# Performance work log

Measured on AMD Instinct MI355X. Metric: run time of the kernel, lower is better.

## Reference

```python
import jax, jax.numpy as jnp
import numpy as np

HEADS = 16
DHEAD = 128
B, S, DMODEL = 2, 2048, 2048


def setup_inputs() -> dict:
    key = jax.random.key(0)
    k1, k2, k3 = jax.random.split(key, 3)
    x = jax.random.normal(k1, (B, S, DMODEL), dtype=jnp.float32)
    # Linear weights, stored as [in, out] so forward is x @ w (no bias).
    w_in = jax.random.normal(k2, (DMODEL, 3 * HEADS * DHEAD), dtype=jnp.float32) * (DMODEL ** -0.5)
    w_out = jax.random.normal(k3, (HEADS * DHEAD, DMODEL), dtype=jnp.float32) * ((HEADS * DHEAD) ** -0.5)
    # Causal mask: True = masked (strictly upper triangular), broadcast over batch & heads.
    mask = jnp.triu(jnp.ones((S, S), dtype=jnp.bool_), k=1)[None, None, :, :]
    return {"x": x, "w_in": w_in, "w_out": w_out, "mask": mask}


def reference(x, w_in, w_out, mask):
    b, s, _ = x.shape
    # Fused QKV projection: [b,s,3*H*dh] -> [b,s,H,3*dh] -> chunk into q,k,v [b,s,H,dh]
    projected = (x @ w_in).reshape(b, s, HEADS, 3 * DHEAD)
    q, k, v = jnp.split(projected, 3, axis=-1)
    # Scores [b,H,l,L], scaled by 1/sqrt(dhead)
    scale = 1.0 / (DHEAD ** 0.5)
    a = jnp.einsum("blhd,bLhd->bhlL", q, k) * scale
    a = jnp.where(mask, -jnp.inf, a)
    a = jax.nn.softmax(a, axis=-1)
    # Weighted values -> [b,l,H,dh] -> flatten heads -> output projection
    out = jnp.einsum("bhlL,bLhd->blhd", a, v).reshape(b, s, HEADS * DHEAD)
    return out @ w_out
```

## Files before the change

kernel.cpp:

```cpp
#include <hip/hip_runtime.h>

#define HD    16
#define DH    128
#define BB    2
#define SS    2048
#define DM    2048
#define NQKV  6144
#define MTOT  4096

typedef short   bfx8  __attribute__((ext_vector_type(8)));
typedef float   f32x4 __attribute__((ext_vector_type(4)));

__device__ __forceinline__ unsigned short f2bf(float f) {
  union { float f; unsigned int u; } c; c.f = f;
  unsigned int u = c.u + 0x7FFFu + ((c.u >> 16) & 1u);
  return (unsigned short)(u >> 16);
}

__device__ __forceinline__ void gload_lds16(const unsigned short* g, unsigned short* l) {
  __builtin_amdgcn_global_load_lds(
      (const __attribute__((address_space(1))) unsigned int*)g,
      (__attribute__((address_space(3))) unsigned int*)l, 16, 0, 0);
}

#define BARS() do { asm volatile("s_waitcnt lgkmcnt(0)" ::: "memory");               \
                    __builtin_amdgcn_sched_barrier(0); __builtin_amdgcn_s_barrier(); \
                    __builtin_amdgcn_sched_barrier(0); } while (0)
#define VMCNT10() do { asm volatile("s_waitcnt vmcnt(10)" ::: "memory"); \
                       __builtin_amdgcn_sched_barrier(0); } while (0)
#define VMCNT8() do { asm volatile("s_waitcnt vmcnt(8)" ::: "memory"); \
                      __builtin_amdgcn_sched_barrier(0); } while (0)

__global__ __launch_bounds__(256) void prep_fused_k(const float* __restrict__ x,
                                                    unsigned short* __restrict__ Xb,
                                                    const float* __restrict__ w_in,
                                                    unsigned short* __restrict__ Wit) {
  __shared__ float t[32][33];
  const int bid = (int)blockIdx.x;
  if (bid < 8192) {
    const int i = bid * 256 + (int)threadIdx.x;
    const float4 v = *(const float4*)(x + (size_t)i * 4);
    ushort4 o;
    o.x = f2bf(v.x); o.y = f2bf(v.y); o.z = f2bf(v.z); o.w = f2bf(v.w);
    *(ushort4*)(Xb + (size_t)i * 4) = o;
    return;
  }
  const int tb = bid - 8192;
  const int c0 = (tb % 192) * 32, r0 = (tb / 192) * 32;
  const int tx = threadIdx.x & 31, ty = threadIdx.x >> 5;
#pragma unroll
  for (int i = 0; i < 4; i++) {
    int r = r0 + ty + i * 8;
    t[ty + i * 8][tx] = w_in[(size_t)r * NQKV + c0 + tx];
  }
  __syncthreads();
#pragma unroll
  for (int i = 0; i < 4; i++) {
    int c = c0 + ty + i * 8;
    Wit[(size_t)c * DM + r0 + tx] = f2bf(t[tx][ty + i * 8]);
  }
}

__global__ __launch_bounds__(256, 2) void gemm128_qkv_k(const unsigned short* __restrict__ A,
                                                        const unsigned short* __restrict__ Bt,
                                                        unsigned short* __restrict__ Qg,
                                                        unsigned short* __restrict__ Kg,
                                                        unsigned short* __restrict__ Vg,
                                                        int K) {
  __shared__ __align__(16) unsigned short Asb[2][128 * 64];
  __shared__ __align__(16) unsigned short Bsb[2][192 * 64];
  const int tid = threadIdx.x;
  const int lane = tid & 63, wid = tid >> 6;
  const int wr = wid >> 1, wc = wid & 1;
  const int cbase = lane & 15, rgrp = lane >> 4;
  const int bid = (int)blockIdx.x;
  const int id = (bid & 7) * 128 + (bid >> 3);
  const int nb = id >> 5, mb = id & 31;
  const size_t m0 = (size_t)mb * 128, n0 = (size_t)nb * 192;
  const int nkt = K >> 6;

#define STAGE_A32(u_, g_) do {                                                          \
    const int uc_ = ((u_) < nkt ? (u_) : (nkt - 1));                                    \
    const int r_ = tid >> 3, s_ = tid & 7;                                              \
    gload_lds16(A + (m0 + (g_) * 32 + r_) * (size_t)K + uc_ * 64 +                      \
                    (((s_ * 16) ^ ((r_ & 7) << 4)) >> 1),                               \
                &Asb[(u_) & 1][(g_) * 2048] + tid * 8); } while (0)
#define STAGE_B32(u_, g_) do {                                                          \
    const int uc_ = ((u_) < nkt ? (u_) : (nkt - 1));                                    \
    const int r_ = tid >> 3, s_ = tid & 7;                                              \
    gload_lds16(Bt + (n0 + (g_) * 32 + r_) * (size_t)K + uc_ * 64 +                     \
                    (((s_ * 16) ^ ((r_ & 7) << 4)) >> 1),                               \
                &Bsb[(u_) & 1][(g_) * 2048] + tid * 8); } while (0)

  const int axor = (cbase & 7) << 4;
  int a_off[2], b_off[2];
#pragma unroll
  for (int ks = 0; ks < 2; ks++) {
    a_off[ks] = ((wr * 64 + cbase) * 128 + ((ks * 64 + rgrp * 16) ^ axor)) >> 1;
    b_off[ks] = ((wc * 96 + cbase) * 128 + ((ks * 64 + rgrp * 16) ^ axor)) >> 1;
  }

#define RD_AALL(dst_, p_) do { _Pragma("unroll")                                         \
    for (int mf_ = 0; mf_ < 4; mf_++) { _Pragma("unroll")                                \
      for (int ks_ = 0; ks_ < 2; ks_++)                                                  \
        dst_[mf_][ks_] = *(const bfx8*)((p_) + a_off[ks_] + mf_ * 1024); } } while (0)
#define RD_BP(dst_, p_, P_) do { _Pragma("unroll")                                       \
    for (int nf_ = 0; nf_ < 2; nf_++) { _Pragma("unroll")                                \
      for (int ks_ = 0; ks_ < 2; ks_++)                                                  \
        dst_[nf_][ks_] = *(const bfx8*)((p_) + b_off[ks_] + (nf_ + (P_)) * 1024); } } while (0)

#define MFMA_P(no_, AF_, BF_) do {                                                       \
    __builtin_amdgcn_s_setprio(1);                                                      \
    _Pragma("unroll")                                                                    \
    for (int mf_ = 0; mf_ < 4; mf_++) { _Pragma("unroll")                                \
      for (int nf_ = 0; nf_ < 2; nf_++) { _Pragma("unroll")                              \
        for (int ks_ = 0; ks_ < 2; ks_++)                                                \
          acc[mf_][nf_ + (no_)] = __builtin_amdgcn_mfma_f32_16x16x32_bf16(               \
              AF_[mf_][ks_], BF_[nf_][ks_], acc[mf_][nf_ + (no_)], 0, 0, 0); } }         \
    __builtin_amdgcn_s_setprio(0); } while (0)

  f32x4 acc[4][6];
  const f32x4 z = {0.f, 0.f, 0.f, 0.f};
#pragma unroll
  for (int mf = 0; mf < 4; mf++)
#pragma unroll
    for (int nf = 0; nf < 6; nf++) acc[mf][nf] = z;

  STAGE_A32(0, 0); STAGE_A32(0, 1); STAGE_A32(0, 2); STAGE_A32(0, 3);
  STAGE_B32(0, 0); STAGE_B32(0, 1); STAGE_B32(0, 2);
  STAGE_B32(0, 3); STAGE_B32(0, 4); STAGE_B32(0, 5);
  STAGE_A32(1, 0); STAGE_A32(1, 1); STAGE_A32(1, 2); STAGE_A32(1, 3);
  STAGE_B32(1, 0); STAGE_B32(1, 1); STAGE_B32(1, 2);
  STAGE_B32(1, 3); STAGE_B32(1, 4); STAGE_B32(1, 5);
  VMCNT10();
  BARS();
  bfx8 aA[4][2], b01A[2][2], aB[4][2], b01B[2][2];
  RD_AALL(aA, &Asb[0][0]);
  RD_BP(b01A, &Bsb[0][0], 0);
  BARS();

#define TILE_BODY(u_, Ac, B01c, An, B01n) do {                                           \
    const unsigned short* Bs_  = &Bsb[(u_) & 1][0];                                      \
    const unsigned short* Asn_ = &Asb[((u_) + 1) & 1][0];                                \
    const unsigned short* Bsn_ = &Bsb[((u_) + 1) & 1][0];                                \
    bfx8 b23[2][2], b45[2][2];                                                           \
        \
                                                             \
    RD_BP(b23, Bs_, 2);                                                                  \
    STAGE_A32((u_) + 2, 0); STAGE_A32((u_) + 2, 1);                                      \
    STAGE_A32((u_) + 2, 2); STAGE_A32((u_) + 2, 3);                                      \
    STAGE_B32((u_) + 2, 0); STAGE_B32((u_) + 2, 3);                                      \
    BARS();                                                                              \
    MFMA_P(0, Ac, B01c);                                                                 \
         \
    RD_BP(b45, Bs_, 4);                                                                  \
    STAGE_B32((u_) + 2, 1); STAGE_B32((u_) + 2, 4);                                      \
    BARS();                                                                              \
    MFMA_P(2, Ac, b23);                                                                  \
        \
                                           \
    STAGE_B32((u_) + 2, 2); STAGE_B32((u_) + 2, 5);                                      \
    VMCNT10();                                                                           \
    BARS();                                                                              \
    RD_AALL(An, Asn_);                                                                   \
    RD_BP(B01n, Bsn_, 0);                                                                \
    MFMA_P(4, Ac, b45);                                                                  \
    BARS();                                                                              \
  } while (0)

#pragma unroll 1
  for (int u = 0; u < nkt; u += 2) {
    TILE_BODY(u,     aA, b01A, aB, b01B);
    TILE_BODY(u + 1, aB, b01B, aA, b01A);
  }
#undef TILE_BODY
#undef STAGE_A32
#undef STAGE_B32

#pragma unroll
  for (int mf = 0; mf < 4; mf++)
#pragma unroll
    for (int nf = 0; nf < 6; nf++) {
      const int nn = (int)n0 + wc * 96 + nf * 16;
      const int h = nn / 384, tt = (nn >> 7) % 3;
      const int d = (nn & 127) + cbase;
      const int row0 = (int)m0 + wr * 64 + mf * 16 + rgrp * 4;
      const int bb = row0 >> 11;
      const int s0 = row0 & 2047;
      if (tt == 2) {
        ushort4 v;
        v.x = f2bf(acc[mf][nf][0]); v.y = f2bf(acc[mf][nf][1]);
        v.z = f2bf(acc[mf][nf][2]); v.w = f2bf(acc[mf][nf][3]);
        *(ushort4*)(Vg + ((size_t)(bb * HD + h) * DH + d) * SS + s0) = v;
      } else {
        unsigned short* dst = (tt == 0 ? Qg : Kg);
#pragma unroll
        for (int r = 0; r < 4; r++)
          dst[((size_t)(bb * HD + h) * SS + s0 + r) * DH + d] = f2bf(acc[mf][nf][r]);
      }
    }
}

__global__ __launch_bounds__(256, 2) void gemm128_out_k(const unsigned short* __restrict__ A,
                                                        const unsigned short* __restrict__ Bt,
                                                        float* __restrict__ C, int K, int ldc) {
  __shared__ __align__(16) unsigned short Asb[2][128 * 64];
  __shared__ __align__(16) unsigned short Bsb[2][128 * 64];
  const int tid = threadIdx.x;
  const int lane = tid & 63, wid = tid >> 6;
  const int wr = wid >> 1, wc = wid & 1;
  const int cbase = lane & 15, rgrp = lane >> 4;
  const int bid = (int)blockIdx.x;
  const int id = (bid & 7) * 64 + (bid >> 3);
  const int nb = id >> 5, mb = id & 31;
  const size_t m0 = (size_t)mb * 128, n0 = (size_t)nb * 128;
  const int nkt = K >> 6;

#define STAGE_AO32(u_, g_) do {                                                         \
    const int uc_ = ((u_) < nkt ? (u_) : (nkt - 1));                                    \
    const int r_ = tid >> 3, s_ = tid & 7;                                              \
    gload_lds16(A + (m0 + (g_) * 32 + r_) * (size_t)K + uc_ * 64 +                      \
                    (((s_ * 16) ^ ((r_ & 7) << 4)) >> 1),                               \
                &Asb[(u_) & 1][(g_) * 2048] + tid * 8); } while (0)
#define STAGE_BO32(u_, g_) do {                                                         \
    const int uc_ = ((u_) < nkt ? (u_) : (nkt - 1));                                    \
    const int r_ = tid >> 3, s_ = tid & 7;                                              \
    gload_lds16(Bt + (n0 + (g_) * 32 + r_) * (size_t)K + uc_ * 64 +                     \
                    (((s_ * 16) ^ ((r_ & 7) << 4)) >> 1),                               \
                &Bsb[(u_) & 1][(g_) * 2048] + tid * 8); } while (0)

  const int axor = (cbase & 7) << 4;
  int a_off[2], b_off[2];
#pragma unroll
  for (int ks = 0; ks < 2; ks++) {
    a_off[ks] = ((wr * 64 + cbase) * 128 + ((ks * 64 + rgrp * 16) ^ axor)) >> 1;
    b_off[ks] = ((wc * 64 + cbase) * 128 + ((ks * 64 + rgrp * 16) ^ axor)) >> 1;
  }

  f32x4 acc[4][4];
  const f32x4 z = {0.f, 0.f, 0.f, 0.f};
#pragma unroll
  for (int mf = 0; mf < 4; mf++)
#pragma unroll
    for (int nf = 0; nf < 4; nf++) acc[mf][nf] = z;

  STAGE_AO32(0, 0); STAGE_AO32(0, 1); STAGE_AO32(0, 2); STAGE_AO32(0, 3);
  STAGE_BO32(0, 0); STAGE_BO32(0, 1); STAGE_BO32(0, 2); STAGE_BO32(0, 3);
  STAGE_AO32(1, 0); STAGE_AO32(1, 1); STAGE_AO32(1, 2); STAGE_AO32(1, 3);
  STAGE_BO32(1, 0); STAGE_BO32(1, 1); STAGE_BO32(1, 2); STAGE_BO32(1, 3);
  VMCNT8();
  BARS();
  bfx8 aA[4][2], b01A[2][2], aB[4][2], b01B[2][2];
  RD_AALL(aA, &Asb[0][0]);
  RD_BP(b01A, &Bsb[0][0], 0);
  BARS();

#define TILE_BODY_Q(u_, Ac, B01c, An, B01n) do {                                         \
    const unsigned short* Bs_  = &Bsb[(u_) & 1][0];                                      \
    const unsigned short* Asn_ = &Asb[((u_) + 1) & 1][0];                                \
    const unsigned short* Bsn_ = &Bsb[((u_) + 1) & 1][0];                                \
    bfx8 b23[2][2];                                                                      \
        \
                                                             \
    RD_BP(b23, Bs_, 2);                                                                  \
    STAGE_AO32((u_) + 2, 0); STAGE_AO32((u_) + 2, 1);                                    \
    STAGE_AO32((u_) + 2, 2); STAGE_AO32((u_) + 2, 3);                                    \
    STAGE_BO32((u_) + 2, 0); STAGE_BO32((u_) + 2, 2);                                    \
    BARS();                                                                              \
    MFMA_P(0, Ac, B01c);                                                                 \
         \
                             \
    STAGE_BO32((u_) + 2, 1); STAGE_BO32((u_) + 2, 3);                                    \
    VMCNT8();                                                                            \
    BARS();                                                                              \
    RD_AALL(An, Asn_);                                                                   \
    RD_BP(B01n, Bsn_, 0);                                                                \
    MFMA_P(2, Ac, b23);                                                                  \
    BARS();                                                                              \
  } while (0)

#pragma unroll 1
  for (int u = 0; u < nkt; u += 2) {
    TILE_BODY_Q(u,     aA, b01A, aB, b01B);
    TILE_BODY_Q(u + 1, aB, b01B, aA, b01A);
  }
#undef TILE_BODY_Q
#undef STAGE_AO32
#undef STAGE_BO32

#pragma unroll
  for (int mf = 0; mf < 4; mf++)
#pragma unroll
    for (int nf = 0; nf < 4; nf++)
#pragma unroll
      for (int r = 0; r < 4; r++) {
        size_t row = m0 + wr * 64 + mf * 16 + rgrp * 4 + r;
        size_t col = n0 + wc * 64 + nf * 16 + cbase;
        C[row * ldc + col] = acc[mf][nf][r];
      }
}

__global__ __launch_bounds__(256) void attn_wot_k(const unsigned short* __restrict__ Qg,
                                                  const unsigned short* __restrict__ Kg,
                                                  const unsigned short* __restrict__ Vg,
                                                  unsigned short* __restrict__ ao,
                                                  const float* __restrict__ w_out,
                                                  unsigned short* __restrict__ Wot) {
  __shared__ __align__(16) unsigned short Klds[2][64 * 128];
  __shared__ __align__(16) unsigned short Vt[2][128 * 64];
  __shared__ __align__(16) unsigned short Plds[4][16 * 64];
  const int tid = threadIdx.x;
  const int bid = (int)blockIdx.x;

  if (bid >= 1024) {
    float* t = (float*)&Klds[0][0];
    const int tb = bid - 1024;
    const int c0 = (tb & 63) * 32, r0 = (tb >> 6) * 32;
    const int tx = tid & 31, ty = tid >> 5;
#pragma unroll
    for (int i = 0; i < 4; i++) {
      int r = r0 + ty + i * 8;
      t[(ty + i * 8) * 33 + tx] = w_out[(size_t)r * DM + c0 + tx];
    }
    __syncthreads();
#pragma unroll
    for (int i = 0; i < 4; i++) {
      int c = c0 + ty + i * 8;
      Wot[(size_t)c * DM + r0 + tx] = f2bf(t[tx * 33 + ty + i * 8]);
    }
    return;
  }

  const int lane = tid & 63, wid = tid >> 6;
  const int cbase = lane & 15, rgrp = lane >> 4;
  const int cx = (cbase & 7) << 4;

  const int bh = (bid & 7) * 4 + ((bid >> 3) & 3);
  const int qt = 31 - (bid >> 5);
  const int b = bh >> 4, h = bh & 15;
  const int qbase = qt * 64;

  const unsigned short* qp0 = Qg + (size_t)(b * HD + h) * SS * DH;
  const unsigned short* kp  = Kg + (size_t)(b * HD + h) * SS * DH;
  const unsigned short* vp  = Vg + (size_t)(b * HD + h) * DH * SS;
  const float scale = 0.08838834764831845f;
  const f32x4 z = {0.f, 0.f, 0.f, 0.f};
  const int qi = qbase + wid * 16 + cbase;

  bfx8 qf[4];
  {
    const unsigned short* qp = qp0 + (size_t)qi * DH;
#pragma unroll
    for (int ks = 0; ks < 4; ks++) qf[ks] = *(const bfx8*)(qp + ks * 32 + rgrp * 8);
  }

  float m_run = -1e30f, l_run = 0.f;
  f32x4 o[8];
#pragma unroll
  for (int mb = 0; mb < 8; mb++) o[mb] = z;

#define STAGE_T(t_, s_) do {                                                        \
    const int kvb_ = (t_) * 64;                                                     \
    _Pragma("unroll")                                                               \
    for (int i_ = 0; i_ < 4; i_++) {                                                \
      int idx_ = i_ * 256 + tid;                                                    \
      int r_ = idx_ >> 4, bo_ = (idx_ & 15) * 16;                                   \
      gload_lds16(kp + (size_t)(kvb_ + r_) * DH + ((bo_ ^ ((r_ & 7) << 4)) >> 1),   \
                  &Klds[s_][idx_ * 8]);                                             \
    }                                                                               \
    _Pragma("unroll")                                                               \
    for (int i_ = 0; i_ < 4; i_++) {                                                \
      int idx_ = i_ * 256 + tid;                                                    \
      int d_ = idx_ >> 3, bo_ = (idx_ & 7) * 16;                                    \
      gload_lds16(vp + (size_t)d_ * SS + kvb_ + ((bo_ ^ ((d_ & 7) << 4)) >> 1),     \
                  &Vt[s_][idx_ * 8]);                                               \
    } } while (0)

  const int ntiles = qt + 1;
  STAGE_T(0, 0);
  __syncthreads();

  for (int t = 0; t < ntiles; ++t) {
    const int sel = t & 1;
    if (t + 1 < ntiles) STAGE_T(t + 1, sel ^ 1);
    const unsigned short* Ks_ = &Klds[sel][0];
    const unsigned short* Vs_ = &Vt[sel][0];
    const int kvb = t * 64;

    f32x4 s[4];
#pragma unroll
    for (int mf = 0; mf < 4; mf++) s[mf] = z;
#pragma unroll
    for (int mf = 0; mf < 4; mf++)
#pragma unroll
      for (int ks = 0; ks < 4; ks++) {
        bfx8 kf = *(const bfx8*)(Ks_ + (((mf * 16 + cbase) * 256 + ((ks * 64 + rgrp * 16) ^ cx)) >> 1));
        s[mf] = __builtin_amdgcn_mfma_f32_16x16x32_bf16(kf, qf[ks], s[mf], 0, 0, 0);
      }

    float sv[4][4];
    const bool diag = (t == ntiles - 1);
#pragma unroll
    for (int mf = 0; mf < 4; mf++)
#pragma unroll
      for (int r = 0; r < 4; r++) {
        float v = s[mf][r] * scale;
        if (diag && (kvb + mf * 16 + rgrp * 4 + r > qi)) v = -1e30f;
        sv[mf][r] = v;
      }
    float tm = sv[0][0];
#pragma unroll
    for (int mf = 0; mf < 4; mf++)
#pragma unroll
      for (int r = 0; r < 4; r++) tm = fmaxf(tm, sv[mf][r]);
    tm = fmaxf(tm, __shfl_xor(tm, 16));
    tm = fmaxf(tm, __shfl_xor(tm, 32));
    const float mnew = fmaxf(m_run, tm);
    float p[4][4];
    float rs = 0.f;
#pragma unroll
    for (int mf = 0; mf < 4; mf++)
#pragma unroll
      for (int r = 0; r < 4; r++) { p[mf][r] = __expf(sv[mf][r] - mnew); rs += p[mf][r]; }
    rs += __shfl_xor(rs, 16);
    rs += __shfl_xor(rs, 32);
    const float alpha = __expf(m_run - mnew);
    l_run = l_run * alpha + rs;
    m_run = mnew;
#pragma unroll
    for (int mb = 0; mb < 8; mb++)
#pragma unroll
      for (int r = 0; r < 4; r++) o[mb][r] *= alpha;

#pragma unroll
    for (int mf = 0; mf < 4; mf++)
#pragma unroll
      for (int rr = 0; rr < 2; rr++) {
        unsigned int pp = (unsigned int)f2bf(p[mf][2 * rr]) |
                          ((unsigned int)f2bf(p[mf][2 * rr + 1]) << 16);
        *(unsigned int*)((char*)&Plds[wid][0] +
                         (cbase * 128 + ((mf * 32 + rgrp * 8 + rr * 4) ^ cx))) = pp;
      }
    bfx8 pf[2];
#pragma unroll
    for (int k2 = 0; k2 < 2; k2++)
      pf[k2] = *(const bfx8*)((const char*)&Plds[wid][0] +
                              (cbase * 128 + ((k2 * 64 + rgrp * 16) ^ cx)));

#pragma unroll
    for (int mb = 0; mb < 8; mb++)
#pragma unroll
      for (int k2 = 0; k2 < 2; k2++) {
        bfx8 vf = *(const bfx8*)(Vs_ + (((mb * 16 + cbase) * 128 + ((k2 * 64 + rgrp * 16) ^ cx)) >> 1));
        o[mb] = __builtin_amdgcn_mfma_f32_16x16x32_bf16(vf, pf[k2], o[mb], 0, 0, 0);
      }
    __syncthreads();
  }
#undef STAGE_T

  const float rinv = 1.0f / l_run;
  unsigned short* aop = ao + ((size_t)(b * SS + qi)) * DM + h * DH + rgrp * 4;
#pragma unroll
  for (int mb = 0; mb < 8; mb++) {
    ushort4 v;
    v.x = f2bf(o[mb][0] * rinv); v.y = f2bf(o[mb][1] * rinv);
    v.z = f2bf(o[mb][2] * rinv); v.w = f2bf(o[mb][3] * rinv);
    *(ushort4*)(aop + mb * 16) = v;
  }
}

extern "C" void kernel_launch(void* const* d_in, const int* in_sizes, int n_in,
                              void* d_out, int out_size, void* d_ws, size_t ws_size,
                              hipStream_t stream) {
  (void)in_sizes; (void)n_in; (void)out_size; (void)ws_size;
  const float* x     = (const float*)d_in[0];
  const float* w_in  = (const float*)d_in[1];
  const float* w_out = (const float*)d_in[2];
  float* out = (float*)d_out;

  char* ws = (char*)d_ws;
  unsigned short* Xb  = (unsigned short*)(ws);
  unsigned short* Wit = (unsigned short*)(ws + (16ull << 20));
  unsigned short* Wot = (unsigned short*)(ws + (40ull << 20));
  unsigned short* Qg  = (unsigned short*)(ws + (48ull << 20));
  unsigned short* Kg  = (unsigned short*)(ws + (64ull << 20));
  unsigned short* Vg  = (unsigned short*)(ws + (80ull << 20));
  unsigned short* AO  = (unsigned short*)(ws + (96ull << 20));

  prep_fused_k<<<20480, 256, 0, stream>>>(x, Xb, w_in, Wit);
  gemm128_qkv_k<<<1024, 256, 0, stream>>>(Xb, Wit, Qg, Kg, Vg, DM);
  attn_wot_k<<<5120, 256, 0, stream>>>(Qg, Kg, Vg, AO, w_out, Wot);
  gemm128_out_k<<<512, 256, 0, stream>>>(AO, Wot, out, DM, DM);
}
```

Baseline: 230.1 us.

## Enlarge QKV GEMM tile to 256x192 with K-step 32 and new swizzle

Replaces the 128x192 QKV projection GEMM with a 256x192 tile per block using a 32-wide K step, halving the grid to 512 blocks. Each wave now holds 8x6 accumulators and reuses each B fragment across eight A fragments, raising arithmetic intensity per LDS read. The LDS layout and XOR swizzle are reworked for 32-element rows, and the pipeline uses one K tile per iteration with a vmcnt(7) wait. The cost is higher register pressure (48 accumulators), fewer blocks for occupancy and load balance, and twice as many barrier-synchronised iterations.

```diff
diff --git a/kernel.cpp b/kernel.cpp
--- a/kernel.cpp
+++ b/kernel.cpp
@@ -26,9 +26,9 @@
 #define BARS() do { asm volatile("s_waitcnt lgkmcnt(0)" ::: "memory");               \
                     __builtin_amdgcn_sched_barrier(0); __builtin_amdgcn_s_barrier(); \
                     __builtin_amdgcn_sched_barrier(0); } while (0)
-#define VMCNT10() do { asm volatile("s_waitcnt vmcnt(10)" ::: "memory"); \
-                       __builtin_amdgcn_sched_barrier(0); } while (0)
 #define VMCNT8() do { asm volatile("s_waitcnt vmcnt(8)" ::: "memory"); \
+                      __builtin_amdgcn_sched_barrier(0); } while (0)
+#define VMCNT7() do { asm volatile("s_waitcnt vmcnt(7)" ::: "memory"); \
                       __builtin_amdgcn_sched_barrier(0); } while (0)
 
 __global__ __launch_bounds__(256) void prep_fused_k(const float* __restrict__ x,
@@ -61,44 +61,126 @@
   }
 }
 
-__global__ __launch_bounds__(256, 2) void gemm128_qkv_k(const unsigned short* __restrict__ A,
+__global__ __launch_bounds__(256, 2) void gemm256_qkv_k(const unsigned short* __restrict__ A,
                                                         const unsigned short* __restrict__ Bt,
                                                         unsigned short* __restrict__ Qg,
                                                         unsigned short* __restrict__ Kg,
                                                         unsigned short* __restrict__ Vg,
                                                         int K) {
-  __shared__ __align__(16) unsigned short Asb[2][128 * 64];
-  __shared__ __align__(16) unsigned short Bsb[2][192 * 64];
+  __shared__ __align__(16) unsigned short Asb[2][256 * 32];
+  __shared__ __align__(16) unsigned short Bsb[2][192 * 32];
   const int tid = threadIdx.x;
   const int lane = tid & 63, wid = tid >> 6;
   const int wr = wid >> 1, wc = wid & 1;
   const int cbase = lane & 15, rgrp = lane >> 4;
   const int bid = (int)blockIdx.x;
-  const int id = (bid & 7) * 128 + (bid >> 3);
-  const int nb = id >> 5, mb = id & 31;
-  const size_t m0 = (size_t)mb * 128, n0 = (size_t)nb * 192;
-  const int nkt = K >> 6;
-
-#define STAGE_A32(u_, g_) do {                                                          \
+  const int id = (bid & 7) * 64 + (bid >> 3);
+  const int nb = id >> 4, mb = id & 15;
+  const size_t m0 = (size_t)mb * 256, n0 = (size_t)nb * 192;
+  const int nkt = K >> 5;
+
+#define QSTAGE_A(u_, g_) do {                                                           \
     const int uc_ = ((u_) < nkt ? (u_) : (nkt - 1));                                    \
-    const int r_ = tid >> 3, s_ = tid & 7;                                              \
-    gload_lds16(A + (m0 + (g_) * 32 + r_) * (size_t)K + uc_ * 64 +                      \
-                    (((s_ * 16) ^ ((r_ & 7) << 4)) >> 1),                               \
+    const int s_ = (tid & 7) ^ ((tid >> 3) & 7);                                        \
+    const int r_ = ((tid >> 3) << 1) | (s_ >> 2);                                       \
+    gload_lds16(A + (m0 + (g_) * 64 + r_) * (size_t)K + uc_ * 32 + ((s_ & 3) << 3),     \
                 &Asb[(u_) & 1][(g_) * 2048] + tid * 8); } while (0)
-#define STAGE_B32(u_, g_) do {                                                          \
+#define QSTAGE_B(u_, g_) do {                                                           \
     const int uc_ = ((u_) < nkt ? (u_) : (nkt - 1));                                    \
-    const int r_ = tid >> 3, s_ = tid & 7;                                              \
-    gload_lds16(Bt + (n0 + (g_) * 32 + r_) * (size_t)K + uc_ * 64 +                     \
-                    (((s_ * 16) ^ ((r_ & 7) << 4)) >> 1),                               \
+    const int s_ = (tid & 7) ^ ((tid >> 3) & 7);                                        \
+    const int r_ = ((tid >> 3) << 1) | (s_ >> 2);                                       \
+    gload_lds16(Bt + (n0 + (g_) * 64 + r_) * (size_t)K + uc_ * 32 + ((s_ & 3) << 3),    \
                 &Bsb[(u_) & 1][(g_) * 2048] + tid * 8); } while (0)
 
-  const int axor = (cbase & 7) << 4;
-  int a_off[2], b_off[2];
-#pragma unroll
-  for (int ks = 0; ks < 2; ks++) {
-    a_off[ks] = ((wr * 64 + cbase) * 128 + ((ks * 64 + rgrp * 16) ^ axor)) >> 1;
-    b_off[ks] = ((wc * 96 + cbase) * 128 + ((ks * 64 + rgrp * 16) ^ axor)) >> 1;
-  }
+  const int rowA = wr * 128 + cbase;
+  const int lineA = rowA >> 1;
+  const int a_off = (lineA * 128 + ((((rowA & 1) << 6) | (rgrp << 4)) ^ ((lineA & 7) << 4))) >> 1;
+  const int rowB = wc * 96 + cbase;
+  const int lineB = rowB >> 1;
+  const int b_off = (lineB * 128 + ((((rowB & 1) << 6) | (rgrp << 4)) ^ ((lineB & 7) << 4))) >> 1;
+
+#define QRD_A(p_) do { _Pragma("unroll")                                                 \
+    for (int mf_ = 0; mf_ < 8; mf_++)                                                    \
+      a[mf_] = *(const bfx8*)((p_) + a_off + mf_ * 512); } while (0)
+#define QRD_B(dst_, p_, P_) do { _Pragma("unroll")                                       \
+    for (int nf_ = 0; nf_ < 2; nf_++)                                                    \
+      dst_[nf_] = *(const bfx8*)((p_) + b_off + (nf_ + (P_)) * 512); } while (0)
+
+#define QMFMA(no_, BF_) do {                                                             \
+    __builtin_amdgcn_s_setprio(1);                                                      \
+    _Pragma("unroll")                                                                    \
+    for (int mf_ = 0; mf_ < 8; mf_++) { _Pragma("unroll")                                \
+      for (int nf_ = 0; nf_ < 2; nf_++)                                                  \
+        acc[mf_][nf_ + (no_)] = __builtin_amdgcn_mfma_f32_16x16x32_bf16(                 \
+            a[mf_], BF_[nf_], acc[mf_][nf_ + (no_)], 0, 0, 0); }                         \
+    __builtin_amdgcn_s_setprio(0); } while (0)
+
+  f32x4 acc[8][6];
+  const f32x4 z = {0.f, 0.f, 0.f, 0.f};
+#pragma unroll
+  for (int mf = 0; mf < 8; mf++)
+#pragma unroll
+    for (int nf = 0; nf < 6; nf++) acc[mf][nf] = z;
+
+  QSTAGE_A(0, 0); QSTAGE_A(0, 1); QSTAGE_A(0, 2); QSTAGE_A(0, 3);
+  QSTAGE_B(0, 0); QSTAGE_B(0, 1); QSTAGE_B(0, 2);
+  QSTAGE_A(1, 0); QSTAGE_A(1, 1); QSTAGE_A(1, 2); QSTAGE_A(1, 3);
+  QSTAGE_B(1, 0); QSTAGE_B(1, 1); QSTAGE_B(1, 2);
+  VMCNT7();
+  BARS();
+  bfx8 a[8], b01[2], b23[2], b45[2];
+  QRD_A(&Asb[0][0]);
+  BARS();
+
+#pragma unroll 1
+  for (int u = 0; u < nkt; ++u) {
+    const unsigned short* Bs_  = &Bsb[u & 1][0];
+    const unsigned short* Asn_ = &Asb[(u + 1) & 1][0];
+    QRD_B(b01, Bs_, 0);
+    QRD_B(b23, Bs_, 2);
+    QSTAGE_A(u + 2, 0); QSTAGE_A(u + 2, 1); QSTAGE_A(u + 2, 2); QSTAGE_A(u + 2, 3);
+    BARS();
+    QMFMA(0, b01);
+    QRD_B(b45, Bs_, 4);
+    QSTAGE_B(u + 2, 0);
+    BARS();
+    QMFMA(2, b23);
+    QSTAGE_B(u + 2, 1); QSTAGE_B(u + 2, 2);
+    VMCNT7();
+    BARS();
+    QMFMA(4, b45);
+    QRD_A(Asn_);
+    BARS();
+  }
+#undef QSTAGE_A
+#undef QSTAGE_B
+#undef QRD_A
+#undef QRD_B
+#undef QMFMA
+
+#pragma unroll
+  for (int mf = 0; mf < 8; mf++)
+#pragma unroll
+    for (int nf = 0; nf < 6; nf++) {
+      const int nn = (int)n0 + wc * 96 + nf * 16;
+      const int h = nn / 384, tt = (nn >> 7) % 3;
+      const int d = (nn & 127) + cbase;
+      const int row0 = (int)m0 + wr * 128 + mf * 16 + rgrp * 4;
+      const int bb = row0 >> 11;
+      const int s0 = row0 & 2047;
+      if (tt == 2) {
+        ushort4 v;
+        v.x = f2bf(acc[mf][nf][0]); v.y = f2bf(acc[mf][nf][1]);
+        v.z = f2bf(acc[mf][nf][2]); v.w = f2bf(acc[mf][nf][3]);
+        *(ushort4*)(Vg + ((size_t)(bb * HD + h) * DH + d) * SS + s0) = v;
+      } else {
+        unsigned short* dst = (tt == 0 ? Qg : Kg);
+#pragma unroll
+        for (int r = 0; r < 4; r++)
+          dst[((size_t)(bb * HD + h) * SS + s0 + r) * DH + d] = f2bf(acc[mf][nf][r]);
+      }
+    }
+}
 
 #define RD_AALL(dst_, p_) do { _Pragma("unroll")                                         \
     for (int mf_ = 0; mf_ < 4; mf_++) { _Pragma("unroll")                                \
@@ -108,7 +190,6 @@
     for (int nf_ = 0; nf_ < 2; nf_++) { _Pragma("unroll")                                \
       for (int ks_ = 0; ks_ < 2; ks_++)                                                  \
         dst_[nf_][ks_] = *(const bfx8*)((p_) + b_off[ks_] + (nf_ + (P_)) * 1024); } } while (0)
-
 #define MFMA_P(no_, AF_, BF_) do {                                                       \
     __builtin_amdgcn_s_setprio(1);                                                      \
     _Pragma("unroll")                                                                    \
@@ -118,88 +199,6 @@
           acc[mf_][nf_ + (no_)] = __builtin_amdgcn_mfma_f32_16x16x32_bf16(               \
               AF_[mf_][ks_], BF_[nf_][ks_], acc[mf_][nf_ + (no_)], 0, 0, 0); } }         \
     __builtin_amdgcn_s_setprio(0); } while (0)
-
-  f32x4 acc[4][6];
-  const f32x4 z = {0.f, 0.f, 0.f, 0.f};
-#pragma unroll
-  for (int mf = 0; mf < 4; mf++)
-#pragma unroll
-    for (int nf = 0; nf < 6; nf++) acc[mf][nf] = z;
-
-  STAGE_A32(0, 0); STAGE_A32(0, 1); STAGE_A32(0, 2); STAGE_A32(0, 3);
-  STAGE_B32(0, 0); STAGE_B32(0, 1); STAGE_B32(0, 2);
-  STAGE_B32(0, 3); STAGE_B32(0, 4); STAGE_B32(0, 5);
-  STAGE_A32(1, 0); STAGE_A32(1, 1); STAGE_A32(1, 2); STAGE_A32(1, 3);
-  STAGE_B32(1, 0); STAGE_B32(1, 1); STAGE_B32(1, 2);
-  STAGE_B32(1, 3); STAGE_B32(1, 4); STAGE_B32(1, 5);
-  VMCNT10();
-  BARS();
-  bfx8 aA[4][2], b01A[2][2], aB[4][2], b01B[2][2];
-  RD_AALL(aA, &Asb[0][0]);
-  RD_BP(b01A, &Bsb[0][0], 0);
-  BARS();
-
-#define TILE_BODY(u_, Ac, B01c, An, B01n) do {                                           \
-    const unsigned short* Bs_  = &Bsb[(u_) & 1][0];                                      \
-    const unsigned short* Asn_ = &Asb[((u_) + 1) & 1][0];                                \
-    const unsigned short* Bsn_ = &Bsb[((u_) + 1) & 1][0];                                \
-    bfx8 b23[2][2], b45[2][2];                                                           \
-        \
-                                                             \
-    RD_BP(b23, Bs_, 2);                                                                  \
-    STAGE_A32((u_) + 2, 0); STAGE_A32((u_) + 2, 1);                                      \
-    STAGE_A32((u_) + 2, 2); STAGE_A32((u_) + 2, 3);                                      \
-    STAGE_B32((u_) + 2, 0); STAGE_B32((u_) + 2, 3);                                      \
-    BARS();                                                                              \
-    MFMA_P(0, Ac, B01c);                                                                 \
-         \
-    RD_BP(b45, Bs_, 4);                                                                  \
-    STAGE_B32((u_) + 2, 1); STAGE_B32((u_) + 2, 4);                                      \
-    BARS();                                                                              \
-    MFMA_P(2, Ac, b23);                                                                  \
-        \
-                                           \
-    STAGE_B32((u_) + 2, 2); STAGE_B32((u_) + 2, 5);                                      \
-    VMCNT10();                                                                           \
-    BARS();                                                                              \
-    RD_AALL(An, Asn_);                                                                   \
-    RD_BP(B01n, Bsn_, 0);                                                                \
-    MFMA_P(4, Ac, b45);                                                                  \
-    BARS();                                                                              \
-  } while (0)
-
-#pragma unroll 1
-  for (int u = 0; u < nkt; u += 2) {
-    TILE_BODY(u,     aA, b01A, aB, b01B);
-    TILE_BODY(u + 1, aB, b01B, aA, b01A);
-  }
-#undef TILE_BODY
-#undef STAGE_A32
-#undef STAGE_B32
-
-#pragma unroll
-  for (int mf = 0; mf < 4; mf++)
-#pragma unroll
-    for (int nf = 0; nf < 6; nf++) {
-      const int nn = (int)n0 + wc * 96 + nf * 16;
-      const int h = nn / 384, tt = (nn >> 7) % 3;
-      const int d = (nn & 127) + cbase;
-      const int row0 = (int)m0 + wr * 64 + mf * 16 + rgrp * 4;
-      const int bb = row0 >> 11;
-      const int s0 = row0 & 2047;
-      if (tt == 2) {
-        ushort4 v;
-        v.x = f2bf(acc[mf][nf][0]); v.y = f2bf(acc[mf][nf][1]);
-        v.z = f2bf(acc[mf][nf][2]); v.w = f2bf(acc[mf][nf][3]);
-        *(ushort4*)(Vg + ((size_t)(bb * HD + h) * DH + d) * SS + s0) = v;
-      } else {
-        unsigned short* dst = (tt == 0 ? Qg : Kg);
-#pragma unroll
-        for (int r = 0; r < 4; r++)
-          dst[((size_t)(bb * HD + h) * SS + s0 + r) * DH + d] = f2bf(acc[mf][nf][r]);
-      }
-    }
-}
 
 __global__ __launch_bounds__(256, 2) void gemm128_out_k(const unsigned short* __restrict__ A,
                                                         const unsigned short* __restrict__ Bt,
@@ -488,7 +487,7 @@
   unsigned short* AO  = (unsigned short*)(ws + (96ull << 20));
 
   prep_fused_k<<<20480, 256, 0, stream>>>(x, Xb, w_in, Wit);
-  gemm128_qkv_k<<<1024, 256, 0, stream>>>(Xb, Wit, Qg, Kg, Vg, DM);
+  gemm256_qkv_k<<<512, 256, 0, stream>>>(Xb, Wit, Qg, Kg, Vg, DM);
   attn_wot_k<<<5120, 256, 0, stream>>>(Qg, Kg, Vg, AO, w_out, Wot);
   gemm128_out_k<<<512, 256, 0, stream>>>(AO, Wot, out, DM, DM);
 }
```

After: 246.3 us. +7.0%, slower.
